# Optimization experiments

Measured on AMD Instinct MI355X. Metric: run time of the kernel, lower is better.

## Reference

```python
import jax, jax.numpy as jnp
import numpy as np

B, T, E, H = 256, 256, 384, 64  # batch, seq (== block_size), embed_dim, head_size

def setup_inputs() -> dict:
    key = jax.random.key(0)
    kx, kq, kk, kv = jax.random.split(key, 4)
    scale = 1.0 / np.sqrt(E)
    return {
        "x": jax.random.normal(kx, (B, T, E), dtype=jnp.float32),
        "Wq": jax.random.normal(kq, (E, H), dtype=jnp.float32) * scale,
        "Wk": jax.random.normal(kk, (E, H), dtype=jnp.float32) * scale,
        "Wv": jax.random.normal(kv, (E, H), dtype=jnp.float32) * scale,
    }

def reference(x, Wq, Wk, Wv):
    # Linear projections (bias-free), faithful to nn.Linear(embed_dim, head_size, bias=False)
    q = jnp.einsum("bte,eh->bth", x, Wq)
    k = jnp.einsum("bte,eh->bth", x, Wk)
    v = jnp.einsum("bte,eh->bth", x, Wv)
    # Scaled QK^T with causal mask, softmax, weighted sum.
    # Dropout is identity in eval mode (reference is deterministic).
    wei = jnp.einsum("bth,bsh->bts", q, k) * (H ** -0.5)  # [B, T, T]
    causal = jnp.tril(jnp.ones((T, T), dtype=bool))
    wei = jnp.where(causal, wei, -jnp.inf)
    wei = jax.nn.softmax(wei, axis=-1)
    out = jnp.einsum("bts,bsh->bth", wei, v)  # [B, T, H]
    return out
```

## Files before the change

kernel.cpp:

```cpp
#include <hip/hip_runtime.h>
#include <hip/hip_bf16.h>

typedef __attribute__((ext_vector_type(8))) short short8;
typedef __attribute__((ext_vector_type(4))) float f32x4;

#define MFMA(a, b, c) __builtin_amdgcn_mfma_f32_16x16x32_bf16((a), (b), (c), 0, 0, 0)

__device__ __forceinline__ unsigned short f2bf(float f) {
  union { float f; unsigned int u; } v; v.f = f;
  unsigned int u = v.u;
  unsigned int r = u + 0x7FFFu + ((u >> 16) & 1u);
  return (unsigned short)(r >> 16);
}

__global__ __launch_bounds__(512) void fused_kernel(
    const float* __restrict__ x, const float* __restrict__ Wq,
    const float* __restrict__ Wk, const float* __restrict__ Wv,
    float* __restrict__ out) {
  extern __shared__ unsigned short sm[];
  unsigned short* Ql = sm;
  unsigned short* Kl = sm + 18432;
  unsigned short* Vl = sm + 36864;
  unsigned short* xl = sm + 53760;
  unsigned short* wl = sm + 64000;

  const int tid = threadIdx.x;
  const int w = tid >> 6, lane = tid & 63, g = lane >> 4, q = lane & 15;
  const int b = blockIdx.x;
  const float* xb = x + (long)b * 256 * 384;

  f32x4 acc[2][12];
  const f32x4 zf = {0.f, 0.f, 0.f, 0.f};
#pragma unroll
  for (int i = 0; i < 2; ++i)
#pragma unroll
    for (int j = 0; j < 12; ++j) acc[i][j] = zf;

  float4 xr[4];
  float4 wr[3];
  const int xk = tid & 31, xc = (tid >> 5) & 15;

  {
    const int k0 = 0;
#pragma unroll
    for (int it = 0; it < 4; ++it) {
      int i = tid + it * 512;
      xr[it] = *(const float4*)&xb[(i >> 3) * 384 + k0 + (i & 7) * 4];
    }
    wr[0] = *(const float4*)&Wq[(k0 + xk) * 64 + xc * 4];
    wr[1] = *(const float4*)&Wk[(k0 + xk) * 64 + xc * 4];
    wr[2] = *(const float4*)&Wv[(k0 + xk) * 64 + xc * 4];
  }

  for (int s = 0; s < 12; ++s) {
    const int k0n = 32 * (s + 1);
    if (s) __syncthreads();
#pragma unroll
    for (int it = 0; it < 4; ++it) {
      int i = tid + it * 512;
      int r = i >> 3, c4 = (i & 7) * 4;
      ushort4 h;
      h.x = f2bf(xr[it].x); h.y = f2bf(xr[it].y);
      h.z = f2bf(xr[it].z); h.w = f2bf(xr[it].w);
      *(ushort4*)&xl[r * 40 + c4] = h;
    }
#pragma unroll
    for (int it = 0; it < 3; ++it) {
      int nb = 64 * it + 4 * xc;
      wl[(nb + 0) * 40 + xk] = f2bf(wr[it].x);
      wl[(nb + 1) * 40 + xk] = f2bf(wr[it].y);
      wl[(nb + 2) * 40 + xk] = f2bf(wr[it].z);
      wl[(nb + 3) * 40 + xk] = f2bf(wr[it].w);
    }
    if (s < 11) {
#pragma unroll
      for (int it = 0; it < 4; ++it) {
        int i = tid + it * 512;
        xr[it] = *(const float4*)&xb[(i >> 3) * 384 + k0n + (i & 7) * 4];
      }
      wr[0] = *(const float4*)&Wq[(k0n + xk) * 64 + xc * 4];
      wr[1] = *(const float4*)&Wk[(k0n + xk) * 64 + xc * 4];
      wr[2] = *(const float4*)&Wv[(k0n + xk) * 64 + xc * 4];
    }
    __syncthreads();
    short8 a0 = *(const short8*)&xl[(32 * w + q) * 40 + g * 8];
    short8 a1 = *(const short8*)&xl[(32 * w + 16 + q) * 40 + g * 8];
#pragma unroll
    for (int ct = 0; ct < 12; ++ct) {
      short8 bfr = *(const short8*)&wl[(16 * ct + q) * 40 + g * 8];
      acc[0][ct] = MFMA(a0, bfr, acc[0][ct]);
      acc[1][ct] = MFMA(a1, bfr, acc[1][ct]);
    }
  }

#pragma unroll
  for (int rt = 0; rt < 2; ++rt) {
    const int mb = 32 * w + 16 * rt + 4 * g;
#pragma unroll
    for (int ct = 0; ct < 12; ++ct) {
      int c = 16 * ct + q;
      unsigned short h0 = f2bf(acc[rt][ct][0]);
      unsigned short h1 = f2bf(acc[rt][ct][1]);
      unsigned short h2 = f2bf(acc[rt][ct][2]);
      unsigned short h3 = f2bf(acc[rt][ct][3]);
      if (ct < 4) {
        Ql[(mb + 0) * 72 + c] = h0; Ql[(mb + 1) * 72 + c] = h1;
        Ql[(mb + 2) * 72 + c] = h2; Ql[(mb + 3) * 72 + c] = h3;
      } else if (ct < 8) {
        int cc = c - 64;
        Kl[(mb + 0) * 72 + cc] = h0; Kl[(mb + 1) * 72 + cc] = h1;
        Kl[(mb + 2) * 72 + cc] = h2; Kl[(mb + 3) * 72 + cc] = h3;
      } else {
        int hh = c - 128;
        ushort4 pk; pk.x = h0; pk.y = h1; pk.z = h2; pk.w = h3;
        *(ushort4*)&Vl[hh * 264 + mb] = pk;
      }
    }
  }
  __syncthreads();

  unsigned short* Pb = xl + w * 640;
  const int tt[2] = {w, 15 - w};
#pragma unroll
  for (int ti = 0; ti < 2; ++ti) {
    const int t = tt[ti];
    short8 aq0 = *(const short8*)&Ql[(16 * t + q) * 72 + g * 8];
    short8 aq1 = *(const short8*)&Ql[(16 * t + q) * 72 + 32 + g * 8];

    f32x4 s[16];
#pragma unroll
    for (int j = 0; j < 16; ++j) {
      if (j <= t) {
        short8 bk0 = *(const short8*)&Kl[(16 * j + q) * 72 + g * 8];
        short8 bk1 = *(const short8*)&Kl[(16 * j + q) * 72 + 32 + g * 8];
        f32x4 sv = MFMA(aq0, bk0, zf);
        sv = MFMA(aq1, bk1, sv);
#pragma unroll
        for (int jr = 0; jr < 4; ++jr) {
          float v = sv[jr] * 0.125f;
          if (j == t && q > 4 * g + jr) v = -1e30f;
          sv[jr] = v;
        }
        s[j] = sv;
      }
    }

    float mrow[4], lrow[4];
#pragma unroll
    for (int jr = 0; jr < 4; ++jr) {
      float m = -1e30f;
#pragma unroll
      for (int j = 0; j < 16; ++j)
        if (j <= t) m = fmaxf(m, s[j][jr]);
      m = fmaxf(m, __shfl_xor(m, 1));
      m = fmaxf(m, __shfl_xor(m, 2));
      m = fmaxf(m, __shfl_xor(m, 4));
      m = fmaxf(m, __shfl_xor(m, 8));
      mrow[jr] = m;
    }
#pragma unroll
    for (int jr = 0; jr < 4; ++jr) {
      float l = 0.0f;
#pragma unroll
      for (int j = 0; j < 16; ++j)
        if (j <= t) {
          float p = __expf(s[j][jr] - mrow[jr]);
          s[j][jr] = p;
          l += p;
        }
      l += __shfl_xor(l, 1);
      l += __shfl_xor(l, 2);
      l += __shfl_xor(l, 4);
      l += __shfl_xor(l, 8);
      lrow[jr] = l;
    }

    f32x4 o[4];
#pragma unroll
    for (int ct = 0; ct < 4; ++ct) o[ct] = zf;
#pragma unroll
    for (int ks = 0; ks < 8; ++ks) {
      if (2 * ks <= t) {
#pragma unroll
        for (int half = 0; half < 2; ++half) {
          int tile = 2 * ks + half;
#pragma unroll
          for (int jr = 0; jr < 4; ++jr) {
            unsigned short pv = 0;
            if (tile <= t) pv = f2bf(s[tile][jr]);
            Pb[(4 * g + jr) * 40 + half * 16 + q] = pv;
          }
        }
        short8 ap = *(const short8*)&Pb[q * 40 + g * 8];
#pragma unroll
        for (int ct = 0; ct < 4; ++ct) {
          short8 bv = *(const short8*)&Vl[(16 * ct + q) * 264 + ks * 32 + g * 8];
          o[ct] = MFMA(ap, bv, o[ct]);
        }
      }
    }

    const long rowbase = (long)b * 256 + 16 * t + 4 * g;
#pragma unroll
    for (int jr = 0; jr < 4; ++jr) {
      float inv = 1.0f / lrow[jr];
#pragma unroll
      for (int ct = 0; ct < 4; ++ct) {
        out[(rowbase + jr) * 64 + 16 * ct + q] = o[ct][jr] * inv;
      }
    }
  }
}

extern "C" void kernel_launch(void* const* d_in, const int* in_sizes, int n_in,
                              void* d_out, int out_size, void* d_ws, size_t ws_size,
                              hipStream_t stream) {
  const float* x  = (const float*)d_in[0];
  const float* Wq = (const float*)d_in[1];
  const float* Wk = (const float*)d_in[2];
  const float* Wv = (const float*)d_in[3];
  float* out = (float*)d_out;

  hipFuncSetAttribute((const void*)fused_kernel,
                      hipFuncAttributeMaxDynamicSharedMemorySize, 143360);
  fused_kernel<<<256, 512, 143360, stream>>>(x, Wq, Wk, Wv, out);
}
```

Baseline: 38.30 us.

## Double-buffer projection staging, pre-convert weights to bf16, use packed conversions and exp2

A separate kernel converts the weights to a transposed bf16 layout once per call, so the fused kernel loads bf16 weight rows with 16-byte loads instead of converting fp32 per tile. The projection K-loop gets double-buffered LDS and two-deep register prefetch, which removes one barrier per step. Rounding to bf16 now uses packed two-at-a-time conversion, and softmax folds log2(e) into the scale so it can use exp2f. LDS usage drops and launch bounds request 2 blocks per CU, though a second kernel launch is added.

```diff
diff --git a/kernel.cpp b/kernel.cpp
--- a/kernel.cpp
+++ b/kernel.cpp
@@ -13,16 +13,27 @@
   return (unsigned short)(r >> 16);
 }
 
-__global__ __launch_bounds__(512) void fused_kernel(
-    const float* __restrict__ x, const float* __restrict__ Wq,
-    const float* __restrict__ Wk, const float* __restrict__ Wv,
+__device__ __forceinline__ unsigned int f2bf2(float a, float b) {
+  __hip_bfloat162 h2 = __float22bfloat162_rn(make_float2(a, b));
+  union { __hip_bfloat162 h; unsigned int u; } cv; cv.h = h2;
+  return cv.u;
+}
+
+__global__ void wconv_kernel(const float* __restrict__ Wq, const float* __restrict__ Wk,
+                             const float* __restrict__ Wv, unsigned short* __restrict__ W3t) {
+  int k = blockIdx.x;
+  int n = threadIdx.x;
+  const float* src = (n < 64) ? Wq : ((n < 128) ? Wk : Wv);
+  W3t[n * 384 + k] = f2bf(src[k * 64 + (n & 63)]);
+}
+
+__global__ __launch_bounds__(512, 2) void fused_kernel(
+    const float* __restrict__ x, const unsigned short* __restrict__ W3t,
     float* __restrict__ out) {
   extern __shared__ unsigned short sm[];
   unsigned short* Ql = sm;
   unsigned short* Kl = sm + 18432;
   unsigned short* Vl = sm + 36864;
-  unsigned short* xl = sm + 53760;
-  unsigned short* wl = sm + 64000;
 
   const int tid = threadIdx.x;
   const int w = tid >> 6, lane = tid & 63, g = lane >> 4, q = lane & 15;
@@ -36,61 +47,68 @@
 #pragma unroll
     for (int j = 0; j < 12; ++j) acc[i][j] = zf;
 
-  float4 xr[4];
-  float4 wr[3];
-  const int xk = tid & 31, xc = (tid >> 5) & 15;
-
-  {
-    const int k0 = 0;
+  float4 xr[2][4];
+  uint4 wr[2][2];
+
+  auto LOAD = [&](int set, int k0) {
 #pragma unroll
     for (int it = 0; it < 4; ++it) {
       int i = tid + it * 512;
-      xr[it] = *(const float4*)&xb[(i >> 3) * 384 + k0 + (i & 7) * 4];
-    }
-    wr[0] = *(const float4*)&Wq[(k0 + xk) * 64 + xc * 4];
-    wr[1] = *(const float4*)&Wk[(k0 + xk) * 64 + xc * 4];
-    wr[2] = *(const float4*)&Wv[(k0 + xk) * 64 + xc * 4];
-  }
-
-  for (int s = 0; s < 12; ++s) {
-    const int k0n = 32 * (s + 1);
-    if (s) __syncthreads();
+      xr[set][it] = *(const float4*)&xb[(i >> 3) * 384 + k0 + (i & 7) * 4];
+    }
+#pragma unroll
+    for (int it = 0; it < 2; ++it) {
+      int c = tid + it * 512;
+      if (c < 768) {
+        int n = c >> 2, koff = (c & 3) * 8;
+        wr[set][it] = *(const uint4*)&W3t[n * 384 + k0 + koff];
+      }
+    }
+  };
+  auto WRITE = [&](int set, int bufofs) {
 #pragma unroll
     for (int it = 0; it < 4; ++it) {
       int i = tid + it * 512;
       int r = i >> 3, c4 = (i & 7) * 4;
-      ushort4 h;
-      h.x = f2bf(xr[it].x); h.y = f2bf(xr[it].y);
-      h.z = f2bf(xr[it].z); h.w = f2bf(xr[it].w);
-      *(ushort4*)&xl[r * 40 + c4] = h;
-    }
-#pragma unroll
-    for (int it = 0; it < 3; ++it) {
-      int nb = 64 * it + 4 * xc;
-      wl[(nb + 0) * 40 + xk] = f2bf(wr[it].x);
-      wl[(nb + 1) * 40 + xk] = f2bf(wr[it].y);
-      wl[(nb + 2) * 40 + xk] = f2bf(wr[it].z);
-      wl[(nb + 3) * 40 + xk] = f2bf(wr[it].w);
-    }
-    if (s < 11) {
-#pragma unroll
-      for (int it = 0; it < 4; ++it) {
-        int i = tid + it * 512;
-        xr[it] = *(const float4*)&xb[(i >> 3) * 384 + k0n + (i & 7) * 4];
-      }
-      wr[0] = *(const float4*)&Wq[(k0n + xk) * 64 + xc * 4];
-      wr[1] = *(const float4*)&Wk[(k0n + xk) * 64 + xc * 4];
-      wr[2] = *(const float4*)&Wv[(k0n + xk) * 64 + xc * 4];
-    }
-    __syncthreads();
-    short8 a0 = *(const short8*)&xl[(32 * w + q) * 40 + g * 8];
-    short8 a1 = *(const short8*)&xl[(32 * w + 16 + q) * 40 + g * 8];
+      uint2 pk;
+      pk.x = f2bf2(xr[set][it].x, xr[set][it].y);
+      pk.y = f2bf2(xr[set][it].z, xr[set][it].w);
+      *(uint2*)&sm[bufofs + r * 40 + c4] = pk;
+    }
+#pragma unroll
+    for (int it = 0; it < 2; ++it) {
+      int c = tid + it * 512;
+      if (c < 768) {
+        int n = c >> 2, koff = (c & 3) * 8;
+        *(uint4*)&sm[bufofs + 10240 + n * 40 + koff] = wr[set][it];
+      }
+    }
+  };
+  auto STEP = [&](int bufofs) {
+    const unsigned short* xlb = sm + bufofs;
+    const unsigned short* wlb = sm + bufofs + 10240;
+    short8 a0 = *(const short8*)&xlb[(32 * w + q) * 40 + g * 8];
+    short8 a1 = *(const short8*)&xlb[(32 * w + 16 + q) * 40 + g * 8];
 #pragma unroll
     for (int ct = 0; ct < 12; ++ct) {
-      short8 bfr = *(const short8*)&wl[(16 * ct + q) * 40 + g * 8];
+      short8 bfr = *(const short8*)&wlb[(16 * ct + q) * 40 + g * 8];
       acc[0][ct] = MFMA(a0, bfr, acc[0][ct]);
       acc[1][ct] = MFMA(a1, bfr, acc[1][ct]);
     }
+  };
+
+  LOAD(0, 0);
+  LOAD(1, 32);
+  WRITE(0, 0);
+  LOAD(0, 64);
+  __syncthreads();
+
+#pragma unroll
+  for (int i = 0; i < 12; ++i) {
+    STEP((i & 1) ? 17920 : 0);
+    if (i < 11) WRITE((i + 1) & 1, ((i + 1) & 1) ? 17920 : 0);
+    if (i < 9)  LOAD((i + 1) & 1, 32 * (i + 3));
+    __syncthreads();
   }
 
 #pragma unroll
@@ -99,10 +117,10 @@
 #pragma unroll
     for (int ct = 0; ct < 12; ++ct) {
       int c = 16 * ct + q;
-      unsigned short h0 = f2bf(acc[rt][ct][0]);
-      unsigned short h1 = f2bf(acc[rt][ct][1]);
-      unsigned short h2 = f2bf(acc[rt][ct][2]);
-      unsigned short h3 = f2bf(acc[rt][ct][3]);
+      unsigned int p01 = f2bf2(acc[rt][ct][0], acc[rt][ct][1]);
+      unsigned int p23 = f2bf2(acc[rt][ct][2], acc[rt][ct][3]);
+      unsigned short h0 = (unsigned short)p01, h1 = (unsigned short)(p01 >> 16);
+      unsigned short h2 = (unsigned short)p23, h3 = (unsigned short)(p23 >> 16);
       if (ct < 4) {
         Ql[(mb + 0) * 72 + c] = h0; Ql[(mb + 1) * 72 + c] = h1;
         Ql[(mb + 2) * 72 + c] = h2; Ql[(mb + 3) * 72 + c] = h3;
@@ -112,14 +130,15 @@
         Kl[(mb + 2) * 72 + cc] = h2; Kl[(mb + 3) * 72 + cc] = h3;
       } else {
         int hh = c - 128;
-        ushort4 pk; pk.x = h0; pk.y = h1; pk.z = h2; pk.w = h3;
-        *(ushort4*)&Vl[hh * 264 + mb] = pk;
+        uint2 pk; pk.x = p01; pk.y = p23;
+        *(uint2*)&Vl[hh * 264 + mb] = pk;
       }
     }
   }
   __syncthreads();
 
-  unsigned short* Pb = xl + w * 640;
+  unsigned short* Pb = sm + 53760 + w * 640;
+  const float SCL = 0.125f * 1.4426950408889634f;
   const int tt[2] = {w, 15 - w};
 #pragma unroll
   for (int ti = 0; ti < 2; ++ti) {
@@ -137,7 +156,7 @@
         sv = MFMA(aq1, bk1, sv);
 #pragma unroll
         for (int jr = 0; jr < 4; ++jr) {
-          float v = sv[jr] * 0.125f;
+          float v = sv[jr] * SCL;
           if (j == t && q > 4 * g + jr) v = -1e30f;
           sv[jr] = v;
         }
@@ -164,7 +183,7 @@
 #pragma unroll
       for (int j = 0; j < 16; ++j)
         if (j <= t) {
-          float p = __expf(s[j][jr] - mrow[jr]);
+          float p = exp2f(s[j][jr] - mrow[jr]);
           s[j][jr] = p;
           l += p;
         }
@@ -184,12 +203,15 @@
 #pragma unroll
         for (int half = 0; half < 2; ++half) {
           int tile = 2 * ks + half;
-#pragma unroll
-          for (int jr = 0; jr < 4; ++jr) {
-            unsigned short pv = 0;
-            if (tile <= t) pv = f2bf(s[tile][jr]);
-            Pb[(4 * g + jr) * 40 + half * 16 + q] = pv;
+          unsigned int p01 = 0, p23 = 0;
+          if (tile <= t) {
+            p01 = f2bf2(s[tile][0], s[tile][1]);
+            p23 = f2bf2(s[tile][2], s[tile][3]);
           }
+          Pb[(4 * g + 0) * 40 + half * 16 + q] = (unsigned short)p01;
+          Pb[(4 * g + 1) * 40 + half * 16 + q] = (unsigned short)(p01 >> 16);
+          Pb[(4 * g + 2) * 40 + half * 16 + q] = (unsigned short)p23;
+          Pb[(4 * g + 3) * 40 + half * 16 + q] = (unsigned short)(p23 >> 16);
         }
         short8 ap = *(const short8*)&Pb[q * 40 + g * 8];
 #pragma unroll
@@ -221,7 +243,11 @@
   const float* Wv = (const float*)d_in[3];
   float* out = (float*)d_out;
 
+  unsigned short* W3t = (unsigned short*)d_ws;
+
   hipFuncSetAttribute((const void*)fused_kernel,
-                      hipFuncAttributeMaxDynamicSharedMemorySize, 143360);
-  fused_kernel<<<256, 512, 143360, stream>>>(x, Wq, Wk, Wv, out);
-}
+                      hipFuncAttributeMaxDynamicSharedMemorySize, 117760);
+
+  wconv_kernel<<<384, 192, 0, stream>>>(Wq, Wk, Wv, W3t);
+  fused_kernel<<<256, 512, 117760, stream>>>(x, W3t, out);
+}
```

Result: slower. 51.28 us (+33.9%).
